# Kernel optimization log

Hardware: AMD Instinct MI355X
Metric: run time of the kernel (lower is better)

## Reference

```python
import jax, jax.numpy as jnp
import numpy as np

N_NODES = 100000
N_EDGES = 1600000
C_IN = 128
C_OUT = 128


def setup_inputs() -> dict:
    key = jax.random.key(0)
    k1, k2, k3, k4, k5, k6 = jax.random.split(key, 6)
    x = jax.random.normal(k1, (N_NODES, C_IN), dtype=jnp.float32)
    rows = jax.random.randint(k2, (N_EDGES,), 0, N_NODES, dtype=jnp.int32)
    cols = jax.random.randint(k3, (N_EDGES,), 0, N_NODES, dtype=jnp.int32)
    vals = jax.random.normal(k4, (N_EDGES,), dtype=jnp.float32)
    # nn.Linear(in, out): W is [out, in], b is [out]
    W = jax.random.normal(k5, (C_OUT, C_IN), dtype=jnp.float32) / np.sqrt(C_IN)
    b = jax.random.normal(k6, (C_OUT,), dtype=jnp.float32) * 0.01
    return {"x": x, "rows": rows, "cols": cols, "vals": vals, "W": W, "b": b}


def reference(x, rows, cols, vals, W, b):
    # out = F @ x  (sparse COO SpMM): out[r] += vals_e * x[cols_e]
    gathered = vals[:, None] * x[cols]              # [E, C_in]
    agg = jax.ops.segment_sum(gathered, rows, num_segments=N_NODES)  # [N, C_in]
    # dense linear projection: agg @ W.T + b
    return jnp.einsum("nc,oc->no", agg, W) + b      # [N, C_out]
```

## Files before the change

### kernel.cpp

```cpp
#include <hip/hip_runtime.h>

#define CH 128
#define MAXB 2048
#define BIN_CHUNK 4096
#define AGG_CAP 2048
#define CAPA 2048

typedef __attribute__((ext_vector_type(8))) short bf16x8;
typedef __attribute__((ext_vector_type(4))) float f32x4;

__device__ inline unsigned short f2bf(float f) {
  unsigned u = __float_as_uint(f);
  return (unsigned short)((u + 0x7FFFu + ((u >> 16) & 1u)) >> 16);
}
__device__ inline float bflo(unsigned u) { return __uint_as_float(u << 16); }
__device__ inline float bfhi(unsigned u) {
  return __uint_as_float(u & 0xFFFF0000u);
}

__global__ void k_init(float4* __restrict__ out, int n4) {
  int i = blockIdx.x * blockDim.x + threadIdx.x;
  int stride = gridDim.x * blockDim.x;
  float4 z = make_float4(0.f, 0.f, 0.f, 0.f);
  for (; i < n4; i += stride) out[i] = z;
}

__global__ void k_scatter(const float* __restrict__ x,
                          const int* __restrict__ rows,
                          const int* __restrict__ cols,
                          const float* __restrict__ vals,
                          float* __restrict__ out, int nEdges) {
  long long total = (long long)nEdges * CH;
  long long stride = (long long)gridDim.x * blockDim.x;
  for (long long i = (long long)blockIdx.x * blockDim.x + threadIdx.x;
       i < total; i += stride) {
    int e = (int)(i >> 7);
    int c = (int)(i & 127);
    unsafeAtomicAdd(out + (((long long)rows[e]) << 7) + c,
                    vals[e] * x[(((long long)cols[e]) << 7) + c]);
  }
}

__device__ __forceinline__ void proj_body(char* Wh, int tid, int pb,
                                          const float* __restrict__ x,
                                          const float* __restrict__ W,
                                          ushort* __restrict__ yh,
                                          int nNodes) {
  for (int i = tid; i < 8192; i += 512) {
    int n = i >> 6, kp = i & 63;
    float2 w2 = *reinterpret_cast<const float2*>(W + n * CH + kp * 2);
    unsigned pk = (unsigned)f2bf(w2.x) | ((unsigned)f2bf(w2.y) << 16);
    int byte = (n * 256 + kp * 4) ^ ((n & 7) << 4);
    *reinterpret_cast<unsigned*>(Wh + byte) = pk;
  }
  __syncthreads();
  int wv = tid >> 6, l = tid & 63;
  int m = l & 15, q = l >> 4;
  int row0 = pb * 128 + wv * 16;
  f32x4 acc[8];
#pragma unroll
  for (int ct = 0; ct < 8; ++ct) acc[ct] = (f32x4){0.f, 0.f, 0.f, 0.f};
#pragma unroll
  for (int ks = 0; ks < 4; ++ks) {
    int arow = row0 + m;
    if (arow >= nNodes) arow = nNodes - 1;
    const float4* xp = reinterpret_cast<const float4*>(
        x + (((long long)arow) << 7) + ks * 32 + q * 8);
    float4 xa = xp[0];
    float4 xb = xp[1];
    bf16x8 af;
    af[0] = (short)f2bf(xa.x);
    af[1] = (short)f2bf(xa.y);
    af[2] = (short)f2bf(xa.z);
    af[3] = (short)f2bf(xa.w);
    af[4] = (short)f2bf(xb.x);
    af[5] = (short)f2bf(xb.y);
    af[6] = (short)f2bf(xb.z);
    af[7] = (short)f2bf(xb.w);
#pragma unroll
    for (int ct = 0; ct < 8; ++ct) {
      int n = ct * 16 + m;
      int byte = (n * 256 + ks * 64 + q * 16) ^ ((n & 7) << 4);
      bf16x8 bfr = *reinterpret_cast<const bf16x8*>(Wh + byte);
      acc[ct] = __builtin_amdgcn_mfma_f32_16x16x32_bf16(af, bfr, acc[ct], 0,
                                                        0, 0);
    }
  }
#pragma unroll
  for (int ct = 0; ct < 8; ++ct) {
#pragma unroll
    for (int r = 0; r < 4; ++r) {
      int orow = row0 + q * 4 + r;
      if (orow < nNodes)
        yh[(((long long)orow) << 7) + ct * 16 + m] = f2bf(acc[ct][r]);
    }
  }
}

__global__ __launch_bounds__(512) void k_binproj(
    const int* __restrict__ rows, const int* __restrict__ cols,
    const float* __restrict__ vals, int* __restrict__ cnt,
    int2* __restrict__ ecv, int nE, int nB, int nBin, int cap,
    const float* __restrict__ x, const float* __restrict__ W,
    ushort* __restrict__ yh, int nNodes) {
  __shared__ char smem[32768];
  int tid = threadIdx.x;
  if ((int)blockIdx.x < nBin) {
    int* lhist = (int*)smem;
    int* lbase = lhist + MAXB;
    int b0 = blockIdx.x * BIN_CHUNK;
    int b1 = min(nE, b0 + BIN_CHUNK);
    for (int i = tid; i < nB; i += 512) lhist[i] = 0;
    __syncthreads();
    for (int i = b0 + tid; i < b1; i += 512)
      atomicAdd(&lhist[rows[i] >> 6], 1);
    __syncthreads();
    for (int t = tid; t < nB; t += 512) {
      int c = lhist[t];
      lbase[t] = c ? atomicAdd(&cnt[t], c) : 0;
    }
    __syncthreads();
    for (int i = b0 + tid; i < b1; i += 512) {
      int r = rows[i];
      int bk = r >> 6;
      int p = atomicAdd(&lbase[bk], 1);
      if (p < cap) {
        unsigned key = ((unsigned)(r & 63) << 25) | (unsigned)cols[i];
        ecv[(long long)bk * cap + p] =
            make_int2((int)key, __float_as_int(vals[i]));
      }
    }
    return;
  }
  proj_body(smem, tid, (int)blockIdx.x - nBin, x, W, yh, nNodes);
}

__global__ __launch_bounds__(512) void k_histproj(
    const int* __restrict__ rows, int* __restrict__ bcnt, int nE, int nB,
    int nHist, const float* __restrict__ x, const float* __restrict__ W,
    ushort* __restrict__ yh, int nNodes) {
  __shared__ char smem[32768];
  int tid = threadIdx.x;
  if ((int)blockIdx.x < nHist) {
    int* lh = (int*)smem;
    for (int i = tid; i < nB; i += 512) lh[i] = 0;
    __syncthreads();
    int stride = nHist * 512;
    for (int i = blockIdx.x * 512 + tid; i < nE; i += stride)
      atomicAdd(&lh[rows[i] >> 6], 1);
    __syncthreads();
    for (int t = tid; t < nB; t += 512)
      if (lh[t]) atomicAdd(&bcnt[t], lh[t]);
    return;
  }
  proj_body(smem, tid, (int)blockIdx.x - nHist, x, W, yh, nNodes);
}

__global__ __launch_bounds__(512) void k_scanB(const int* __restrict__ bcnt,
                                               int* __restrict__ bptr,
                                               int* __restrict__ cursor,
                                               int nB) {
  __shared__ int s[512];
  int t = threadIdx.x;
  int v[4];
  int sum = 0;
#pragma unroll
  for (int k = 0; k < 4; ++k) {
    int idx = t * 4 + k;
    v[k] = (idx < nB) ? bcnt[idx] : 0;
    sum += v[k];
  }
  s[t] = sum;
  __syncthreads();
  for (int off = 1; off < 512; off <<= 1) {
    int add = (t >= off) ? s[t - off] : 0;
    __syncthreads();
    s[t] += add;
    __syncthreads();
  }
  int run = s[t] - sum;
#pragma unroll
  for (int k = 0; k < 4; ++k) {
    int idx = t * 4 + k;
    if (idx < nB) {
      bptr[idx] = run;
      cursor[idx] = run;
    }
    run += v[k];
  }
  if (t == 511) bptr[nB] = run;
}

__global__ __launch_bounds__(512) void k_bin(const int* __restrict__ rows,
                                             const int* __restrict__ cols,
                                             const float* __restrict__ vals,
                                             int* __restrict__ cursor,
                                             int2* __restrict__ ecv, int nE,
                                             int nB) {
  __shared__ int lhist[MAXB];
  __shared__ int lbase[MAXB];
  int tid = threadIdx.x;
  int b0 = blockIdx.x * BIN_CHUNK;
  int b1 = min(nE, b0 + BIN_CHUNK);
  for (int i = tid; i < nB; i += 512) lhist[i] = 0;
  __syncthreads();
  for (int i = b0 + tid; i < b1; i += 512) atomicAdd(&lhist[rows[i] >> 6], 1);
  __syncthreads();
  for (int t = tid; t < nB; t += 512) {
    int c = lhist[t];
    lbase[t] = c ? atomicAdd(&cursor[t], c) : 0;
  }
  __syncthreads();
  for (int i = b0 + tid; i < b1; i += 512) {
    int r = rows[i];
    int bk = r >> 6;
    int p = atomicAdd(&lbase[bk], 1);
    unsigned key = ((unsigned)(r & 63) << 25) | (unsigned)cols[i];
    ecv[p] = make_int2((int)key, __float_as_int(vals[i]));
  }
}

__global__ __launch_bounds__(256) void k_agg_bf16(
    const ushort* __restrict__ yh, const int2* __restrict__ ecv,
    const int* __restrict__ meta, const float* __restrict__ bias,
    float* __restrict__ out, int nNodes, int cap) {
  __shared__ unsigned skey[AGG_CAP];
  __shared__ float sval[AGG_CAP];
  __shared__ int rcnt[64];
  __shared__ int roff[64];
  __shared__ int rcur[64];
  int tid = threadIdx.x;
  int wave = tid >> 6, lane = tid & 63;
  int c0 = lane << 1;
  int b = blockIdx.x;
  long long e0;
  int count;
  if (cap > 0) {
    e0 = (long long)b * cap;
    count = min(meta[b], cap);
  } else {
    int p0 = meta[b];
    e0 = p0;
    count = meta[b + 1] - p0;
  }
  float2 acc[16];
#pragma unroll
  for (int i = 0; i < 16; ++i) acc[i] = make_float2(0.f, 0.f);

  for (int base = 0; base < count; base += AGG_CAP) {
    int cnt = min(AGG_CAP, count - base);
    if (tid < 64) rcnt[tid] = 0;
    __syncthreads();
    for (int i = tid; i < cnt; i += 256)
      atomicAdd(&rcnt[((unsigned)ecv[e0 + base + i].x) >> 25], 1);
    __syncthreads();
    if (wave == 0) {
      int a = rcnt[lane];
      int pref = a;
#pragma unroll
      for (int d = 1; d < 64; d <<= 1) {
        int t = __shfl_up(pref, d);
        if (lane >= d) pref += t;
      }
      roff[lane] = pref - a;
      rcur[lane] = pref - a;
    }
    __syncthreads();
    for (int i = tid; i < cnt; i += 256) {
      int2 e = ecv[e0 + base + i];
      unsigned key = (unsigned)e.x;
      int lr = (int)(key >> 25);
      int p = atomicAdd(&rcur[lr], 1);
      skey[p] = key & 0x1FFFFFFu;
      sval[p] = __int_as_float(e.y);
    }
    __syncthreads();
#pragma unroll
    for (int i = 0; i < 16; ++i) {
      int lr = (wave << 4) + i;
      int j0 = roff[lr];
      int j1 = j0 + rcnt[lr];
      int j = j0;
      for (; j + 8 <= j1; j += 8) {
        unsigned cv[8];
        float vv[8];
        unsigned uu[8];
#pragma unroll
        for (int t = 0; t < 8; ++t) {
          cv[t] = skey[j + t];
          vv[t] = sval[j + t];
        }
#pragma unroll
        for (int t = 0; t < 8; ++t)
          uu[t] = *reinterpret_cast<const unsigned*>(
              yh + (((long long)cv[t]) << 7) + c0);
#pragma unroll
        for (int t = 0; t < 8; ++t) {
          acc[i].x = fmaf(vv[t], bflo(uu[t]), acc[i].x);
          acc[i].y = fmaf(vv[t], bfhi(uu[t]), acc[i].y);
        }
      }
      for (; j + 4 <= j1; j += 4) {
        unsigned cv[4];
        float vv[4];
        unsigned uu[4];
#pragma unroll
        for (int t = 0; t < 4; ++t) {
          cv[t] = skey[j + t];
          vv[t] = sval[j + t];
        }
#pragma unroll
        for (int t = 0; t < 4; ++t)
          uu[t] = *reinterpret_cast<const unsigned*>(
              yh + (((long long)cv[t]) << 7) + c0);
#pragma unroll
        for (int t = 0; t < 4; ++t) {
          acc[i].x = fmaf(vv[t], bflo(uu[t]), acc[i].x);
          acc[i].y = fmaf(vv[t], bfhi(uu[t]), acc[i].y);
        }
      }
      for (; j < j1; ++j) {
        int col = (int)skey[j];
        float v = sval[j];
        unsigned u = *reinterpret_cast<const unsigned*>(
            yh + (((long long)col) << 7) + c0);
        acc[i].x = fmaf(v, bflo(u), acc[i].x);
        acc[i].y = fmaf(v, bfhi(u), acc[i].y);
      }
    }
    __syncthreads();
  }
  const float2 bv = *reinterpret_cast<const float2*>(bias + c0);
  int row0 = b << 6;
#pragma unroll
  for (int i = 0; i < 16; ++i) {
    int r = row0 + (wave << 4) + i;
    if (r < nNodes) {
      float2 res = make_float2(acc[i].x + bv.x, acc[i].y + bv.y);
      *reinterpret_cast<float2*>(out + (((long long)r) << 7) + c0) = res;
    }
  }
}

__global__ __launch_bounds__(256) void k_agg_f32(
    const float* __restrict__ x, const int2* __restrict__ ecv,
    const int* __restrict__ bptr, float* __restrict__ out, int nNodes) {
  __shared__ unsigned skey[AGG_CAP];
  __shared__ float sval[AGG_CAP];
  __shared__ int rcnt[64];
  __shared__ int roff[64];
  __shared__ int rcur[64];
  int tid = threadIdx.x;
  int wave = tid >> 6, lane = tid & 63;
  int c0 = lane << 1;
  int b = blockIdx.x;
  int e0 = bptr[b];
  int count = bptr[b + 1] - e0;
  float2 acc[16];
#pragma unroll
  for (int i = 0; i < 16; ++i) acc[i] = make_float2(0.f, 0.f);
  for (int base = 0; base < count; base += AGG_CAP) {
    int cnt = min(AGG_CAP, count - base);
    if (tid < 64) rcnt[tid] = 0;
    __syncthreads();
    for (int i = tid; i < cnt; i += 256)
      atomicAdd(&rcnt[((unsigned)ecv[e0 + base + i].x) >> 25], 1);
    __syncthreads();
    if (wave == 0) {
      int a = rcnt[lane];
      int pref = a;
#pragma unroll
      for (int d = 1; d < 64; d <<= 1) {
        int t = __shfl_up(pref, d);
        if (lane >= d) pref += t;
      }
      roff[lane] = pref - a;
      rcur[lane] = pref - a;
    }
    __syncthreads();
    for (int i = tid; i < cnt; i += 256) {
      int2 e = ecv[e0 + base + i];
      unsigned key = (unsigned)e.x;
      int lr = (int)(key >> 25);
      int p = atomicAdd(&rcur[lr], 1);
      skey[p] = key & 0x1FFFFFFu;
      sval[p] = __int_as_float(e.y);
    }
    __syncthreads();
#pragma unroll
    for (int i = 0; i < 16; ++i) {
      int lr = (wave << 4) + i;
      int j0 = roff[lr];
      int j1 = j0 + rcnt[lr];
      for (int j = j0; j < j1; ++j) {
        int col = (int)skey[j];
        float v = sval[j];
        const float2 xv =
            *reinterpret_cast<const float2*>(x + (((long long)col) << 7) + c0);
        acc[i].x = fmaf(v, xv.x, acc[i].x);
        acc[i].y = fmaf(v, xv.y, acc[i].y);
      }
    }
    __syncthreads();
  }
  int row0 = b << 6;
#pragma unroll
  for (int i = 0; i < 16; ++i) {
    int r = row0 + (wave << 4) + i;
    if (r < nNodes)
      *reinterpret_cast<float2*>(out + (((long long)r) << 7) + c0) = acc[i];
  }
}

#define PRJ_ROWS 64
__global__ __launch_bounds__(256) void k_project(float* __restrict__ out,
                                                 const float* __restrict__ W,
                                                 const float* __restrict__ bias,
                                                 int nNodes) {
  __shared__ float sWt[CH * CH];
  __shared__ float sA[8 * 68];
  int tid = threadIdx.x;
  int og = tid & 31, rg = tid >> 5;
  for (int idx = tid; idx < CH * CH; idx += 256) {
    int o = idx >> 7, c = idx & 127;
    sWt[(c * CH + o) ^ ((c & 31) << 2)] = W[idx];
  }
  int row0 = blockIdx.x * PRJ_ROWS;
  float acc[8][4];
#pragma unroll
  for (int i = 0; i < 8; ++i)
#pragma unroll
    for (int j = 0; j < 4; ++j) acc[i][j] = 0.f;
  int sr = tid >> 2;
  int skc = (tid & 3) << 1;
  __syncthreads();
  for (int kk = 0; kk < CH; kk += 8) {
    float2 av = make_float2(0.f, 0.f);
    int grow = row0 + sr;
    if (grow < nNodes)
      av = *reinterpret_cast<const float2*>(out + (((long long)grow) << 7) +
                                            kk + skc);
    sA[skc * 68 + sr] = av.x;
    sA[(skc + 1) * 68 + sr] = av.y;
    __syncthreads();
#pragma unroll
    for (int kc = 0; kc < 8; ++kc) {
      int c = kk + kc;
      const float4 w4 = *reinterpret_cast<const float4*>(
          &sWt[(c * CH + (og << 2)) ^ ((c & 31) << 2)]);
      const float4 a0 =
          *reinterpret_cast<const float4*>(&sA[kc * 68 + (rg << 3)]);
      const float4 a1 =
          *reinterpret_cast<const float4*>(&sA[kc * 68 + (rg << 3) + 4]);
      acc[0][0] = fmaf(a0.x, w4.x, acc[0][0]);
      acc[0][1] = fmaf(a0.x, w4.y, acc[0][1]);
      acc[0][2] = fmaf(a0.x, w4.z, acc[0][2]);
      acc[0][3] = fmaf(a0.x, w4.w, acc[0][3]);
      acc[1][0] = fmaf(a0.y, w4.x, acc[1][0]);
      acc[1][1] = fmaf(a0.y, w4.y, acc[1][1]);
      acc[1][2] = fmaf(a0.y, w4.z, acc[1][2]);
      acc[1][3] = fmaf(a0.y, w4.w, acc[1][3]);
      acc[2][0] = fmaf(a0.z, w4.x, acc[2][0]);
      acc[2][1] = fmaf(a0.z, w4.y, acc[2][1]);
      acc[2][2] = fmaf(a0.z, w4.z, acc[2][2]);
      acc[2][3] = fmaf(a0.z, w4.w, acc[2][3]);
      acc[3][0] = fmaf(a0.w, w4.x, acc[3][0]);
      acc[3][1] = fmaf(a0.w, w4.y, acc[3][1]);
      acc[3][2] = fmaf(a0.w, w4.z, acc[3][2]);
      acc[3][3] = fmaf(a0.w, w4.w, acc[3][3]);
      acc[4][0] = fmaf(a1.x, w4.x, acc[4][0]);
      acc[4][1] = fmaf(a1.x, w4.y, acc[4][1]);
      acc[4][2] = fmaf(a1.x, w4.z, acc[4][2]);
      acc[4][3] = fmaf(a1.x, w4.w, acc[4][3]);
      acc[5][0] = fmaf(a1.y, w4.x, acc[5][0]);
      acc[5][1] = fmaf(a1.y, w4.y, acc[5][1]);
      acc[5][2] = fmaf(a1.y, w4.z, acc[5][2]);
      acc[5][3] = fmaf(a1.y, w4.w, acc[5][3]);
      acc[6][0] = fmaf(a1.z, w4.x, acc[6][0]);
      acc[6][1] = fmaf(a1.z, w4.y, acc[6][1]);
      acc[6][2] = fmaf(a1.z, w4.z, acc[6][2]);
      acc[6][3] = fmaf(a1.z, w4.w, acc[6][3]);
      acc[7][0] = fmaf(a1.w, w4.x, acc[7][0]);
      acc[7][1] = fmaf(a1.w, w4.y, acc[7][1]);
      acc[7][2] = fmaf(a1.w, w4.z, acc[7][2]);
      acc[7][3] = fmaf(a1.w, w4.w, acc[7][3]);
    }
    __syncthreads();
  }
  int o0 = og << 2;
  const float4 bv = *reinterpret_cast<const float4*>(&bias[o0]);
#pragma unroll
  for (int i = 0; i < 8; ++i) {
    int r = row0 + (rg << 3) + i;
    if (r < nNodes) {
      float4 res = make_float4(acc[i][0] + bv.x, acc[i][1] + bv.y,
                               acc[i][2] + bv.z, acc[i][3] + bv.w);
      *reinterpret_cast<float4*>(out + (((long long)r) << 7) + o0) = res;
    }
  }
}

extern "C" void kernel_launch(void* const* d_in, const int* in_sizes, int n_in,
                              void* d_out, int out_size, void* d_ws,
                              size_t ws_size, hipStream_t stream) {
  const float* x = (const float*)d_in[0];
  const int* rows = (const int*)d_in[1];
  const int* cols = (const int*)d_in[2];
  const float* vals = (const float*)d_in[3];
  const float* W = (const float*)d_in[4];
  const float* b = (const float*)d_in[5];
  float* out = (float*)d_out;

  int nEdges = in_sizes[1];
  int nNodes = in_sizes[0] / CH;
  int nPrjBlocks = (nNodes + PRJ_ROWS - 1) / PRJ_ROWS;
  int nB2 = (nNodes + 63) >> 6;
  int nBinBlocks = (nEdges + BIN_CHUNK - 1) / BIN_CHUNK;
  int nPrj128 = (nNodes + 127) / 128;
  int nHist = 256;

  size_t ecvOffA = ((size_t)nB2 + 1) & ~(size_t)1;
  size_t yhOffA = ecvOffA + (size_t)nB2 * 2 * CAPA;
  size_t needA = (yhOffA + (size_t)nNodes * 64) * 4;
  size_t headB = (size_t)(3 * nB2 + 1);
  size_t ecvOffB = (headB + 1) & ~(size_t)1;
  size_t yhOffB = ecvOffB + 2 * (size_t)nEdges;
  size_t needB = (yhOffB + (size_t)nNodes * 64) * 4;
  size_t needMid = (ecvOffB + 2 * (size_t)nEdges) * 4;

  bool shapeOk = (nB2 <= MAXB) && (nNodes < (1 << 25));
  int* wsI = (int*)d_ws;

  if (!shapeOk || ws_size < needMid) {
    hipLaunchKernelGGL(k_init, dim3(2048), dim3(256), 0, stream, (float4*)out,
                       out_size / 4);
    hipLaunchKernelGGL(k_scatter, dim3(4096), dim3(256), 0, stream, x, rows,
                       cols, vals, out, nEdges);
    hipLaunchKernelGGL(k_project, dim3(nPrjBlocks), dim3(256), 0, stream, out,
                       W, b, nNodes);
    return;
  }

  if (ws_size >= needA) {
    int* cnt = wsI;
    int2* ecv = (int2*)(wsI + ecvOffA);
    ushort* yh = (ushort*)(wsI + yhOffA);
    hipMemsetAsync(cnt, 0, (size_t)nB2 * 4, stream);
    hipLaunchKernelGGL(k_binproj, dim3(nBinBlocks + nPrj128), dim3(512), 0,
                       stream, rows, cols, vals, cnt, ecv, nEdges, nB2,
                       nBinBlocks, CAPA, x, W, yh, nNodes);
    hipLaunchKernelGGL(k_agg_bf16, dim3(nB2), dim3(256), 0, stream, yh, ecv,
                       cnt, b, out, nNodes, CAPA);
  } else if (ws_size >= needB) {
    int* bptr = wsI;
    int* cursor = bptr + (nB2 + 1);
    int* bcnt = cursor + nB2;
    int2* ecv = (int2*)(wsI + ecvOffB);
    ushort* yh = (ushort*)(wsI + yhOffB);
    hipMemsetAsync(bcnt, 0, (size_t)nB2 * 4, stream);
    hipLaunchKernelGGL(k_histproj, dim3(nHist + nPrj128), dim3(512), 0, stream,
                       rows, bcnt, nEdges, nB2, nHist, x, W, yh, nNodes);
    hipLaunchKernelGGL(k_scanB, dim3(1), dim3(512), 0, stream, bcnt, bptr,
                       cursor, nB2);
    hipLaunchKernelGGL(k_bin, dim3(nBinBlocks), dim3(512), 0, stream, rows,
                       cols, vals, cursor, ecv, nEdges, nB2);
    hipLaunchKernelGGL(k_agg_bf16, dim3(nB2), dim3(256), 0, stream, yh, ecv,
                       bptr, b, out, nNodes, 0);
  } else {
    int* bptr = wsI;
    int* cursor = bptr + (nB2 + 1);
    int* bcnt = cursor + nB2;
    int2* ecv = (int2*)(wsI + ecvOffB);
    hipMemsetAsync(bcnt, 0, (size_t)nB2 * 4, stream);
    hipLaunchKernelGGL(k_histproj, dim3(nHist), dim3(512), 0, stream, rows,
                       bcnt, nEdges, nB2, nHist, x, W, (ushort*)nullptr,
                       nNodes);
    hipLaunchKernelGGL(k_scanB, dim3(1), dim3(512), 0, stream, bcnt, bptr,
                       cursor, nB2);
    hipLaunchKernelGGL(k_bin, dim3(nBinBlocks), dim3(512), 0, stream, rows,
                       cols, vals, cursor, ecv, nEdges, nB2);
    hipLaunchKernelGGL(k_agg_f32, dim3(nB2), dim3(256), 0, stream, x, ecv,
                       bptr, out, nNodes);
    hipLaunchKernelGGL(k_project, dim3(nPrjBlocks), dim3(256), 0, stream, out,
                       W, b, nNodes);
  }
}
```

Measured before the change: 153.0 us.

## Use 128-row buckets with 512-thread aggregation and padded edge lists

Doubles the row bucket size from 64 to 128 rows. Binning, histogram, scan and aggregation kernels are resized to match, and the aggregation kernels now run 8 waves per block. In the bf16 aggregation path, each row's edge list in shared memory is padded to a multiple of 8 with zero-valued entries, so the 4-wide and scalar tail loops are removed and only the 8-wide gather loop remains. This halves the number of aggregation blocks and avoids divergent tail handling, at the cost of larger shared memory per block (which may lower occupancy), some wasted gathers of row 0 for padding, and a larger fixed per-bucket capacity.

After: 143.3 us. 6.3% less time.

```diff
diff --git a/kernel.cpp b/kernel.cpp
--- a/kernel.cpp
+++ b/kernel.cpp
@@ -1,10 +1,11 @@
 #include <hip/hip_runtime.h>
 
 #define CH 128
-#define MAXB 2048
+#define MAXB 1024
 #define BIN_CHUNK 4096
-#define AGG_CAP 2048
-#define CAPA 2048
+#define AGG_CAP 4096
+#define PADCAP 5120
+#define CAPA 4096
 
 typedef __attribute__((ext_vector_type(8))) short bf16x8;
 typedef __attribute__((ext_vector_type(4))) float f32x4;
@@ -113,7 +114,7 @@
     for (int i = tid; i < nB; i += 512) lhist[i] = 0;
     __syncthreads();
     for (int i = b0 + tid; i < b1; i += 512)
-      atomicAdd(&lhist[rows[i] >> 6], 1);
+      atomicAdd(&lhist[rows[i] >> 7], 1);
     __syncthreads();
     for (int t = tid; t < nB; t += 512) {
       int c = lhist[t];
@@ -122,10 +123,10 @@
     __syncthreads();
     for (int i = b0 + tid; i < b1; i += 512) {
       int r = rows[i];
-      int bk = r >> 6;
+      int bk = r >> 7;
       int p = atomicAdd(&lbase[bk], 1);
       if (p < cap) {
-        unsigned key = ((unsigned)(r & 63) << 25) | (unsigned)cols[i];
+        unsigned key = ((unsigned)(r & 127) << 25) | (unsigned)cols[i];
         ecv[(long long)bk * cap + p] =
             make_int2((int)key, __float_as_int(vals[i]));
       }
@@ -147,7 +148,7 @@
     __syncthreads();
     int stride = nHist * 512;
     for (int i = blockIdx.x * 512 + tid; i < nE; i += stride)
-      atomicAdd(&lh[rows[i] >> 6], 1);
+      atomicAdd(&lh[rows[i] >> 7], 1);
     __syncthreads();
     for (int t = tid; t < nB; t += 512)
       if (lh[t]) atomicAdd(&bcnt[t], lh[t]);
@@ -156,11 +157,11 @@
   proj_body(smem, tid, (int)blockIdx.x - nHist, x, W, yh, nNodes);
 }
 
-__global__ __launch_bounds__(512) void k_scanB(const int* __restrict__ bcnt,
+__global__ __launch_bounds__(256) void k_scanB(const int* __restrict__ bcnt,
                                                int* __restrict__ bptr,
                                                int* __restrict__ cursor,
                                                int nB) {
-  __shared__ int s[512];
+  __shared__ int s[256];
   int t = threadIdx.x;
   int v[4];
   int sum = 0;
@@ -172,7 +173,7 @@
   }
   s[t] = sum;
   __syncthreads();
-  for (int off = 1; off < 512; off <<= 1) {
+  for (int off = 1; off < 256; off <<= 1) {
     int add = (t >= off) ? s[t - off] : 0;
     __syncthreads();
     s[t] += add;
@@ -188,7 +189,7 @@
     }
     run += v[k];
   }
-  if (t == 511) bptr[nB] = run;
+  if (t == 255) bptr[nB] = run;
 }
 
 __global__ __launch_bounds__(512) void k_bin(const int* __restrict__ rows,
@@ -204,7 +205,7 @@
   int b1 = min(nE, b0 + BIN_CHUNK);
   for (int i = tid; i < nB; i += 512) lhist[i] = 0;
   __syncthreads();
-  for (int i = b0 + tid; i < b1; i += 512) atomicAdd(&lhist[rows[i] >> 6], 1);
+  for (int i = b0 + tid; i < b1; i += 512) atomicAdd(&lhist[rows[i] >> 7], 1);
   __syncthreads();
   for (int t = tid; t < nB; t += 512) {
     int c = lhist[t];
@@ -213,22 +214,22 @@
   __syncthreads();
   for (int i = b0 + tid; i < b1; i += 512) {
     int r = rows[i];
-    int bk = r >> 6;
+    int bk = r >> 7;
     int p = atomicAdd(&lbase[bk], 1);
-    unsigned key = ((unsigned)(r & 63) << 25) | (unsigned)cols[i];
+    unsigned key = ((unsigned)(r & 127) << 25) | (unsigned)cols[i];
     ecv[p] = make_int2((int)key, __float_as_int(vals[i]));
   }
 }
 
-__global__ __launch_bounds__(256) void k_agg_bf16(
+__global__ __launch_bounds__(512) void k_agg_bf16(
     const ushort* __restrict__ yh, const int2* __restrict__ ecv,
     const int* __restrict__ meta, const float* __restrict__ bias,
     float* __restrict__ out, int nNodes, int cap) {
-  __shared__ unsigned skey[AGG_CAP];
-  __shared__ float sval[AGG_CAP];
-  __shared__ int rcnt[64];
-  __shared__ int roff[64];
-  __shared__ int rcur[64];
+  __shared__ unsigned skey[PADCAP];
+  __shared__ float sval[PADCAP];
+  __shared__ int rcnt[CH];
+  __shared__ int roff[CH];
+  __shared__ int rcur[CH];
   int tid = threadIdx.x;
   int wave = tid >> 6, lane = tid & 63;
   int c0 = lane << 1;
@@ -249,24 +250,29 @@
 
   for (int base = 0; base < count; base += AGG_CAP) {
     int cnt = min(AGG_CAP, count - base);
-    if (tid < 64) rcnt[tid] = 0;
-    __syncthreads();
-    for (int i = tid; i < cnt; i += 256)
+    if (tid < CH) rcnt[tid] = 0;
+    __syncthreads();
+    for (int i = tid; i < cnt; i += 512)
       atomicAdd(&rcnt[((unsigned)ecv[e0 + base + i].x) >> 25], 1);
     __syncthreads();
     if (wave == 0) {
-      int a = rcnt[lane];
-      int pref = a;
+      int a = (rcnt[lane * 2] + 7) & ~7;
+      int bq = (rcnt[lane * 2 + 1] + 7) & ~7;
+      int s = a + bq;
+      int pref = s;
 #pragma unroll
       for (int d = 1; d < 64; d <<= 1) {
         int t = __shfl_up(pref, d);
         if (lane >= d) pref += t;
       }
-      roff[lane] = pref - a;
-      rcur[lane] = pref - a;
-    }
-    __syncthreads();
-    for (int i = tid; i < cnt; i += 256) {
+      int excl = pref - s;
+      roff[lane * 2] = excl;
+      rcur[lane * 2] = excl;
+      roff[lane * 2 + 1] = excl + a;
+      rcur[lane * 2 + 1] = excl + a;
+    }
+    __syncthreads();
+    for (int i = tid; i < cnt; i += 512) {
       int2 e = ecv[e0 + base + i];
       unsigned key = (unsigned)e.x;
       int lr = (int)(key >> 25);
@@ -275,13 +281,21 @@
       sval[p] = __int_as_float(e.y);
     }
     __syncthreads();
+    if (tid < CH) {
+      int j = roff[tid] + rcnt[tid];
+      int jend = roff[tid] + ((rcnt[tid] + 7) & ~7);
+      for (; j < jend; ++j) {
+        skey[j] = 0;
+        sval[j] = 0.f;
+      }
+    }
+    __syncthreads();
 #pragma unroll
     for (int i = 0; i < 16; ++i) {
       int lr = (wave << 4) + i;
       int j0 = roff[lr];
-      int j1 = j0 + rcnt[lr];
-      int j = j0;
-      for (; j + 8 <= j1; j += 8) {
+      int j1 = j0 + ((rcnt[lr] + 7) & ~7);
+      for (int j = j0; j < j1; j += 8) {
         unsigned cv[8];
         float vv[8];
         unsigned uu[8];
@@ -300,38 +314,11 @@
           acc[i].y = fmaf(vv[t], bfhi(uu[t]), acc[i].y);
         }
       }
-      for (; j + 4 <= j1; j += 4) {
-        unsigned cv[4];
-        float vv[4];
-        unsigned uu[4];
-#pragma unroll
-        for (int t = 0; t < 4; ++t) {
-          cv[t] = skey[j + t];
-          vv[t] = sval[j + t];
-        }
-#pragma unroll
-        for (int t = 0; t < 4; ++t)
-          uu[t] = *reinterpret_cast<const unsigned*>(
-              yh + (((long long)cv[t]) << 7) + c0);
-#pragma unroll
-        for (int t = 0; t < 4; ++t) {
-          acc[i].x = fmaf(vv[t], bflo(uu[t]), acc[i].x);
-          acc[i].y = fmaf(vv[t], bfhi(uu[t]), acc[i].y);
-        }
-      }
-      for (; j < j1; ++j) {
-        int col = (int)skey[j];
-        float v = sval[j];
-        unsigned u = *reinterpret_cast<const unsigned*>(
-            yh + (((long long)col) << 7) + c0);
-        acc[i].x = fmaf(v, bflo(u), acc[i].x);
-        acc[i].y = fmaf(v, bfhi(u), acc[i].y);
-      }
     }
     __syncthreads();
   }
   const float2 bv = *reinterpret_cast<const float2*>(bias + c0);
-  int row0 = b << 6;
+  int row0 = b << 7;
 #pragma unroll
   for (int i = 0; i < 16; ++i) {
     int r = row0 + (wave << 4) + i;
@@ -342,14 +329,14 @@
   }
 }
 
-__global__ __launch_bounds__(256) void k_agg_f32(
+__global__ __launch_bounds__(512) void k_agg_f32(
     const float* __restrict__ x, const int2* __restrict__ ecv,
     const int* __restrict__ bptr, float* __restrict__ out, int nNodes) {
   __shared__ unsigned skey[AGG_CAP];
   __shared__ float sval[AGG_CAP];
-  __shared__ int rcnt[64];
-  __shared__ int roff[64];
-  __shared__ int rcur[64];
+  __shared__ int rcnt[CH];
+  __shared__ int roff[CH];
+  __shared__ int rcur[CH];
   int tid = threadIdx.x;
   int wave = tid >> 6, lane = tid & 63;
   int c0 = lane << 1;
@@ -361,24 +348,29 @@
   for (int i = 0; i < 16; ++i) acc[i] = make_float2(0.f, 0.f);
   for (int base = 0; base < count; base += AGG_CAP) {
     int cnt = min(AGG_CAP, count - base);
-    if (tid < 64) rcnt[tid] = 0;
-    __syncthreads();
-    for (int i = tid; i < cnt; i += 256)
+    if (tid < CH) rcnt[tid] = 0;
+    __syncthreads();
+    for (int i = tid; i < cnt; i += 512)
       atomicAdd(&rcnt[((unsigned)ecv[e0 + base + i].x) >> 25], 1);
     __syncthreads();
     if (wave == 0) {
-      int a = rcnt[lane];
-      int pref = a;
+      int a = rcnt[lane * 2];
+      int bq = rcnt[lane * 2 + 1];
+      int s = a + bq;
+      int pref = s;
 #pragma unroll
       for (int d = 1; d < 64; d <<= 1) {
         int t = __shfl_up(pref, d);
         if (lane >= d) pref += t;
       }
-      roff[lane] = pref - a;
-      rcur[lane] = pref - a;
-    }
-    __syncthreads();
-    for (int i = tid; i < cnt; i += 256) {
+      int excl = pref - s;
+      roff[lane * 2] = excl;
+      rcur[lane * 2] = excl;
+      roff[lane * 2 + 1] = excl + a;
+      rcur[lane * 2 + 1] = excl + a;
+    }
+    __syncthreads();
+    for (int i = tid; i < cnt; i += 512) {
       int2 e = ecv[e0 + base + i];
       unsigned key = (unsigned)e.x;
       int lr = (int)(key >> 25);
@@ -403,7 +395,7 @@
     }
     __syncthreads();
   }
-  int row0 = b << 6;
+  int row0 = b << 7;
 #pragma unroll
   for (int i = 0; i < 16; ++i) {
     int r = row0 + (wave << 4) + i;
@@ -514,21 +506,21 @@
   int nEdges = in_sizes[1];
   int nNodes = in_sizes[0] / CH;
   int nPrjBlocks = (nNodes + PRJ_ROWS - 1) / PRJ_ROWS;
-  int nB2 = (nNodes + 63) >> 6;
+  int nB = (nNodes + 127) >> 7;
   int nBinBlocks = (nEdges + BIN_CHUNK - 1) / BIN_CHUNK;
   int nPrj128 = (nNodes + 127) / 128;
   int nHist = 256;
 
-  size_t ecvOffA = ((size_t)nB2 + 1) & ~(size_t)1;
-  size_t yhOffA = ecvOffA + (size_t)nB2 * 2 * CAPA;
+  size_t ecvOffA = ((size_t)nB + 1) & ~(size_t)1;
+  size_t yhOffA = ecvOffA + (size_t)nB * 2 * CAPA;
   size_t needA = (yhOffA + (size_t)nNodes * 64) * 4;
-  size_t headB = (size_t)(3 * nB2 + 1);
+  size_t headB = (size_t)(3 * nB + 1);
   size_t ecvOffB = (headB + 1) & ~(size_t)1;
   size_t yhOffB = ecvOffB + 2 * (size_t)nEdges;
   size_t needB = (yhOffB + (size_t)nNodes * 64) * 4;
   size_t needMid = (ecvOffB + 2 * (size_t)nEdges) * 4;
 
-  bool shapeOk = (nB2 <= MAXB) && (nNodes < (1 << 25));
+  bool shapeOk = (nB <= MAXB) && (nNodes < (1 << 25));
   int* wsI = (int*)d_ws;
 
   if (!shapeOk || ws_size < needMid) {
@@ -545,41 +537,41 @@
     int* cnt = wsI;
     int2* ecv = (int2*)(wsI + ecvOffA);
     ushort* yh = (ushort*)(wsI + yhOffA);
-    hipMemsetAsync(cnt, 0, (size_t)nB2 * 4, stream);
+    hipMemsetAsync(cnt, 0, (size_t)nB * 4, stream);
     hipLaunchKernelGGL(k_binproj, dim3(nBinBlocks + nPrj128), dim3(512), 0,
-                       stream, rows, cols, vals, cnt, ecv, nEdges, nB2,
+                       stream, rows, cols, vals, cnt, ecv, nEdges, nB,
                        nBinBlocks, CAPA, x, W, yh, nNodes);
-    hipLaunchKernelGGL(k_agg_bf16, dim3(nB2), dim3(256), 0, stream, yh, ecv,
+    hipLaunchKernelGGL(k_agg_bf16, dim3(nB), dim3(512), 0, stream, yh, ecv,
                        cnt, b, out, nNodes, CAPA);
   } else if (ws_size >= needB) {
     int* bptr = wsI;
-    int* cursor = bptr + (nB2 + 1);
-    int* bcnt = cursor + nB2;
+    int* cursor = bptr + (nB + 1);
+    int* bcnt = cursor + nB;
     int2* ecv = (int2*)(wsI + ecvOffB);
     ushort* yh = (ushort*)(wsI + yhOffB);
-    hipMemsetAsync(bcnt, 0, (size_t)nB2 * 4, stream);
+    hipMemsetAsync(bcnt, 0, (size_t)nB * 4, stream);
     hipLaunchKernelGGL(k_histproj, dim3(nHist + nPrj128), dim3(512), 0, stream,
-                       rows, bcnt, nEdges, nB2, nHist, x, W, yh, nNodes);
-    hipLaunchKernelGGL(k_scanB, dim3(1), dim3(512), 0, stream, bcnt, bptr,
-                       cursor, nB2);
+                       rows, bcnt, nEdges, nB, nHist, x, W, yh, nNodes);
+    hipLaunchKernelGGL(k_scanB, dim3(1), dim3(256), 0, stream, bcnt, bptr,
+                       cursor, nB);
     hipLaunchKernelGGL(k_bin, dim3(nBinBlocks), dim3(512), 0, stream, rows,
-                       cols, vals, cursor, ecv, nEdges, nB2);
-    hipLaunchKernelGGL(k_agg_bf16, dim3(nB2), dim3(256), 0, stream, yh, ecv,
+                       cols, vals, cursor, ecv, nEdges, nB);
+    hipLaunchKernelGGL(k_agg_bf16, dim3(nB), dim3(512), 0, stream, yh, ecv,
                        bptr, b, out, nNodes, 0);
   } else {
     int* bptr = wsI;
-    int* cursor = bptr + (nB2 + 1);
-    int* bcnt = cursor + nB2;
+    int* cursor = bptr + (nB + 1);
+    int* bcnt = cursor + nB;
     int2* ecv = (int2*)(wsI + ecvOffB);
-    hipMemsetAsync(bcnt, 0, (size_t)nB2 * 4, stream);
+    hipMemsetAsync(bcnt, 0, (size_t)nB * 4, stream);
     hipLaunchKernelGGL(k_histproj, dim3(nHist), dim3(512), 0, stream, rows,
-                       bcnt, nEdges, nB2, nHist, x, W, (ushort*)nullptr,
+                       bcnt, nEdges, nB, nHist, x, W, (ushort*)nullptr,
                        nNodes);
-    hipLaunchKernelGGL(k_scanB, dim3(1), dim3(512), 0, stream, bcnt, bptr,
-                       cursor, nB2);
+    hipLaunchKernelGGL(k_scanB, dim3(1), dim3(256), 0, stream, bcnt, bptr,
+                       cursor, nB);
     hipLaunchKernelGGL(k_bin, dim3(nBinBlocks), dim3(512), 0, stream, rows,
-                       cols, vals, cursor, ecv, nEdges, nB2);
-    hipLaunchKernelGGL(k_agg_f32, dim3(nB2), dim3(256), 0, stream, x, ecv,
+                       cols, vals, cursor, ecv, nEdges, nB);
+    hipLaunchKernelGGL(k_agg_f32, dim3(nB), dim3(512), 0, stream, x, ecv,
                        bptr, out, nNodes);
     hipLaunchKernelGGL(k_project, dim3(nPrjBlocks), dim3(256), 0, stream, out,
                        W, b, nNodes);
```
